# Performance work log

Measured on AMD Instinct MI355X. Metric: run time of the kernel, lower is better.

Reference implementation:

```python
import jax, jax.numpy as jnp
import numpy as np

B, S, D = 4, 1024, 1024
H = 16
HD = D // H  # 64
LN_EPS = 1e-5


def setup_inputs() -> dict:
    key = jax.random.key(0)
    ks = jax.random.split(key, 12)
    s = 1.0 / np.sqrt(D)
    return {
        "x": jax.random.normal(ks[0], (B, S, D), dtype=jnp.float32),
        "wq": jax.random.normal(ks[1], (D, D), dtype=jnp.float32) * s,
        "bq": jnp.zeros((D,), dtype=jnp.float32),
        "wk": jax.random.normal(ks[2], (D, D), dtype=jnp.float32) * s,
        "bk": jnp.zeros((D,), dtype=jnp.float32),
        "wv": jax.random.normal(ks[3], (D, D), dtype=jnp.float32) * s,
        "bv": jnp.zeros((D,), dtype=jnp.float32),
        "wl": jax.random.normal(ks[4], (D, D), dtype=jnp.float32) * s,
        "bl": jnp.zeros((D,), dtype=jnp.float32),
        "ln_g": jnp.ones((D,), dtype=jnp.float32),
        "ln_b": jnp.zeros((D,), dtype=jnp.float32),
    }


def _heads(t):
    # [B,S,D] -> [B,H,S,HD]
    return t.reshape(B, S, H, HD).transpose(0, 2, 1, 3)


def reference(x, wq, bq, wk, bk, wv, bv, wl, bl, ln_g, ln_b):
    q = _heads(x @ wq.T + bq)
    k = _heads(x @ wk.T + bk)
    v = _heads(x @ wv.T + bv)
    score = jnp.einsum("bhqd,bhkd->bhqk", q, k)
    # NOTE: unusual order — softmax first, THEN divide by sqrt(head_size)
    score = jax.nn.softmax(score, axis=-1) / jnp.sqrt(jnp.float32(HD))
    att = jnp.einsum("bhqk,bhkd->bhqd", score, v)
    att = att.transpose(0, 2, 1, 3).reshape(B, S, D)
    # residual added BEFORE the output linear
    y = (att + x) @ wl.T + bl
    # LayerNorm over last dim
    mu = jnp.mean(y, axis=-1, keepdims=True)
    var = jnp.mean(jnp.square(y - mu), axis=-1, keepdims=True)
    out = (y - mu) * jax.lax.rsqrt(var + LN_EPS) * ln_g + ln_b
    # dropout is identity in eval mode
    return out
```

## Files before the change

### kernel.cpp

```cpp
#include <hip/hip_runtime.h>
#include <cstdint>
#include <cstddef>

typedef __bf16 bf16;
typedef __bf16 bf16x4_t __attribute__((ext_vector_type(4)));
typedef __bf16 bf16x8_t __attribute__((ext_vector_type(8)));
typedef float f32x4_t __attribute__((ext_vector_type(4)));

#define DEV static __device__ __forceinline__

DEV void gload16(const void* g, void* l) {
  __builtin_amdgcn_global_load_lds((const __attribute__((address_space(1))) void*)g,
                                   (__attribute__((address_space(3))) void*)l, 16, 0, 0);
}

DEV f32x4_t mfma16(bf16x8_t a, bf16x8_t b, f32x4_t c) {
  return __builtin_amdgcn_mfma_f32_16x16x32_bf16(a, b, c, 0, 0, 0);
}

__global__ __launch_bounds__(256) void k_convert(
    const float* __restrict__ x, const float* __restrict__ wq,
    const float* __restrict__ wk, const float* __restrict__ wv,
    const float* __restrict__ wl,
    bf16* __restrict__ xb, bf16* __restrict__ wqkvb, bf16* __restrict__ wlb) {
  const size_t M1 = (size_t)1 << 20;
  size_t i = ((size_t)blockIdx.x * 256 + threadIdx.x) * 4;
  const float* src; bf16* dst; size_t off;
  if (i < 4 * M1)      { src = x;  dst = xb;           off = i; }
  else if (i < 5 * M1) { src = wq; dst = wqkvb;        off = i - 4 * M1; }
  else if (i < 6 * M1) { src = wk; dst = wqkvb + M1;   off = i - 5 * M1; }
  else if (i < 7 * M1) { src = wv; dst = wqkvb + 2*M1; off = i - 6 * M1; }
  else                 { src = wl; dst = wlb;          off = i - 7 * M1; }
  f32x4_t v = *(const f32x4_t*)&src[off];
  bf16x4_t o;
  o[0] = (bf16)v[0]; o[1] = (bf16)v[1]; o[2] = (bf16)v[2]; o[3] = (bf16)v[3];
  *(bf16x4_t*)&dst[off] = o;
}

DEV void gemm_mainloop(const bf16* __restrict__ A, const bf16* __restrict__ B,
                       int m0, int n0,
                       bf16 (*lA)[128 * 64], bf16 (*lB)[128 * 64],
                       f32x4_t (&acc)[4][4]) {
  const int tid = threadIdx.x, wave = tid >> 6, lane = tid & 63;
  const int wm = (wave >> 1) * 64, wn = (wave & 1) * 64;
  const int fr = lane & 15, fg = lane >> 4;
  const int rowoff = wave * 8 + (lane >> 3);
  const int csw = (((lane & 7) ^ (lane >> 3)) << 3);

  auto STAGE = [&](int buf, int kt) {
#pragma unroll
    for (int i = 0; i < 4; ++i) {
      gload16(A + (size_t)(m0 + i * 32 + rowoff) * 1024 + kt * 64 + csw,
              &lA[buf][(i * 32 + wave * 8) * 64]);
      gload16(B + (size_t)(n0 + i * 32 + rowoff) * 1024 + kt * 64 + csw,
              &lB[buf][(i * 32 + wave * 8) * 64]);
    }
  };

  auto COMPUTE = [&](int buf) {
    bf16x8_t af[4][2], bfr[4][2];
#pragma unroll
    for (int mi = 0; mi < 4; ++mi)
#pragma unroll
      for (int ks = 0; ks < 2; ++ks) {
        const int r = wm + mi * 16 + fr;
        af[mi][ks] = *(const bf16x8_t*)
            &lA[buf][r * 64 + ((((ks << 2) + fg) ^ (fr & 7)) << 3)];
      }
#pragma unroll
    for (int ni = 0; ni < 4; ++ni)
#pragma unroll
      for (int ks = 0; ks < 2; ++ks) {
        const int r = wn + ni * 16 + fr;
        bfr[ni][ks] = *(const bf16x8_t*)
            &lB[buf][r * 64 + ((((ks << 2) + fg) ^ (fr & 7)) << 3)];
      }
    __builtin_amdgcn_s_setprio(1);
#pragma unroll
    for (int ks = 0; ks < 2; ++ks)
#pragma unroll
      for (int mi = 0; mi < 4; ++mi)
#pragma unroll
        for (int ni = 0; ni < 4; ++ni)
          acc[mi][ni] = mfma16(af[mi][ks], bfr[ni][ks], acc[mi][ni]);
    __builtin_amdgcn_s_setprio(0);
  };

  STAGE(0, 0);
  STAGE(1, 1);
  for (int t = 0; t < 15; ++t) {
    asm volatile("s_waitcnt vmcnt(8)" ::: "memory");
    __builtin_amdgcn_s_barrier();
    COMPUTE(t & 1);
    __builtin_amdgcn_s_barrier();
    if (t < 14) STAGE(t & 1, t + 2);
  }
  asm volatile("s_waitcnt vmcnt(0)" ::: "memory");
  __builtin_amdgcn_s_barrier();
  COMPUTE(1);
}

__global__ __launch_bounds__(256, 2) void k_gemm_qkv(
    const bf16* __restrict__ W, const bf16* __restrict__ Xb,
    const float* __restrict__ bq, const float* __restrict__ bk,
    const float* __restrict__ bv,
    bf16* __restrict__ Q, bf16* __restrict__ Kc, bf16* __restrict__ VT) {
  __shared__ alignas(16) bf16 lA[2][128 * 64];
  __shared__ alignas(16) bf16 lB[2][128 * 64];
  const f32x4_t vzero = {0.f, 0.f, 0.f, 0.f};
  f32x4_t acc[4][4];
#pragma unroll
  for (int a = 0; a < 4; ++a)
#pragma unroll
    for (int c = 0; c < 4; ++c) acc[a][c] = vzero;
  const int m0 = blockIdx.x * 128, n0 = blockIdx.y * 128;
  gemm_mainloop(W, Xb, m0, n0, lA, lB, acc);

  const int tid = threadIdx.x, wave = tid >> 6, lane = tid & 63;
  const int wm = (wave >> 1) * 64, wn = (wave & 1) * 64;
  const int fr = lane & 15, fg = lane >> 4;
  const int region = m0 >> 10;
  const float* bp = (region == 0) ? bq : ((region == 1) ? bk : bv);
  bf16* QK = (region == 0) ? Q : Kc;
#pragma unroll
  for (int mi = 0; mi < 4; ++mi) {
    const int f = (m0 & 1023) + wm + mi * 16 + fg * 4;
    const int h = f >> 6, d = f & 63;
#pragma unroll
    for (int ni = 0; ni < 4; ++ni) {
      const int t = n0 + wn + ni * 16 + fr;
      const int b = t >> 10, s = t & 1023;
      const int bh = b * 16 + h;
      f32x4_t v = acc[mi][ni];
      if (region < 2) {
        bf16x4_t o;
#pragma unroll
        for (int j = 0; j < 4; ++j) o[j] = (bf16)(v[j] + bp[f + j]);
        *(bf16x4_t*)&QK[((size_t)bh * 1024 + s) * 64 + d] = o;
      } else {
#pragma unroll
        for (int j = 0; j < 4; ++j)
          VT[((size_t)bh * 64 + d + j) * 1024 + s] = (bf16)(v[j] + bp[f + j]);
      }
    }
  }
}

#define P_STRIDE 72

__global__ __launch_bounds__(256) void k_attn(
    const bf16* __restrict__ Q, const bf16* __restrict__ K,
    const bf16* __restrict__ VT, const float* __restrict__ X,
    bf16* __restrict__ ATTB) {
  __shared__ alignas(16) bf16 lK[2][64 * 64];
  __shared__ alignas(16) bf16 lV[2][64 * 64];
  __shared__ alignas(16) bf16 lP[4][32 * P_STRIDE];
  const int tid = threadIdx.x, wave = tid >> 6, lane = tid & 63;
  const int bh = blockIdx.x, qt = blockIdx.y;
  const int q0 = qt * 128 + wave * 32;
  const int fr = lane & 15, fg = lane >> 4;
  const int rx = (fr & 7) << 3;
  const f32x4_t vzero = {0.f, 0.f, 0.f, 0.f};

  bf16x8_t qf[2][2];
#pragma unroll
  for (int mi = 0; mi < 2; ++mi)
#pragma unroll
    for (int ks = 0; ks < 2; ++ks)
      qf[mi][ks] = *(const bf16x8_t*)
          &Q[((size_t)bh * 1024 + q0 + mi * 16 + fr) * 64 + ks * 32 + fg * 8];

  f32x4_t oacc[2][4];
  f32x4_t lsum[2];
#pragma unroll
  for (int mi = 0; mi < 2; ++mi) {
    lsum[mi] = vzero;
#pragma unroll
    for (int dj = 0; dj < 4; ++dj) oacc[mi][dj] = vzero;
  }

  const int srow = lane >> 3;
  const int scolsw = (((lane & 7) ^ srow) * 8);

  auto STAGE = [&](int buf, int kv) {
#pragma unroll
    for (int i = 0; i < 2; ++i) {
      const int c = wave * 2 + i;
      gload16(&K[((size_t)bh * 1024 + kv * 64 + c * 8 + srow) * 64 + scolsw],
              &lK[buf][c * 512]);
      gload16(&VT[((size_t)bh * 64 + c * 8 + srow) * 1024 + kv * 64 + scolsw],
              &lV[buf][c * 512]);
    }
  };

  STAGE(0, 0);
  __syncthreads();

  for (int kv = 0; kv < 16; ++kv) {
    const int cur = kv & 1;
    if (kv < 15) STAGE(cur ^ 1, kv + 1);

    bf16x8_t kb[4][2];
#pragma unroll
    for (int nj = 0; nj < 4; ++nj)
#pragma unroll
      for (int ks = 0; ks < 2; ++ks) {
        const int r = nj * 16 + fr;
        kb[nj][ks] = *(const bf16x8_t*)&lK[cur][r * 64 + ((ks * 32 + fg * 8) ^ rx)];
      }
    f32x4_t s[2][4];
#pragma unroll
    for (int mi = 0; mi < 2; ++mi)
#pragma unroll
      for (int nj = 0; nj < 4; ++nj) {
        f32x4_t z = vzero;
#pragma unroll
        for (int ks = 0; ks < 2; ++ks) z = mfma16(qf[mi][ks], kb[nj][ks], z);
        s[mi][nj] = z;
      }

#pragma unroll
    for (int mi = 0; mi < 2; ++mi)
#pragma unroll
      for (int nj = 0; nj < 4; ++nj)
#pragma unroll
        for (int j = 0; j < 4; ++j) {
          float p = __expf(s[mi][nj][j]);
          lsum[mi][j] += p;
          lP[wave][(mi * 16 + fg * 4 + j) * P_STRIDE + nj * 16 + fr] = (bf16)p;
        }

    bf16x8_t vb[4][2], pa[2][2];
#pragma unroll
    for (int dj = 0; dj < 4; ++dj)
#pragma unroll
      for (int ks = 0; ks < 2; ++ks) {
        const int r = dj * 16 + fr;
        vb[dj][ks] = *(const bf16x8_t*)&lV[cur][r * 64 + ((ks * 32 + fg * 8) ^ rx)];
      }
#pragma unroll
    for (int mi = 0; mi < 2; ++mi)
#pragma unroll
      for (int ks = 0; ks < 2; ++ks)
        pa[mi][ks] = *(const bf16x8_t*)
            &lP[wave][(mi * 16 + fr) * P_STRIDE + ks * 32 + fg * 8];
#pragma unroll
    for (int mi = 0; mi < 2; ++mi)
#pragma unroll
      for (int dj = 0; dj < 4; ++dj)
#pragma unroll
        for (int ks = 0; ks < 2; ++ks)
          oacc[mi][dj] = mfma16(pa[mi][ks], vb[dj][ks], oacc[mi][dj]);

    __syncthreads();
  }

#pragma unroll
  for (int mi = 0; mi < 2; ++mi)
#pragma unroll
    for (int m = 1; m < 16; m <<= 1)
#pragma unroll
      for (int j = 0; j < 4; ++j)
        lsum[mi][j] += __shfl_xor(lsum[mi][j], m);

  const int b = bh >> 4, h = bh & 15;
#pragma unroll
  for (int mi = 0; mi < 2; ++mi)
#pragma unroll
    for (int dj = 0; dj < 4; ++dj)
#pragma unroll
      for (int j = 0; j < 4; ++j) {
        const int s_ = q0 + mi * 16 + fg * 4 + j;
        const int d_ = dj * 16 + fr;
        const size_t tok = (size_t)b * 1024 + s_;
        const size_t fidx = (size_t)h * 64 + d_;
        float val = oacc[mi][dj][j] / lsum[mi][j] * 0.125f + X[tok * 1024 + fidx];
        ATTB[tok * 1024 + fidx] = (bf16)val;
      }
}

__global__ __launch_bounds__(256, 2) void k_gemm_out(
    const bf16* __restrict__ Wl, const bf16* __restrict__ Ax,
    const float* __restrict__ bl, float* __restrict__ Y) {
  __shared__ alignas(16) bf16 lA[2][128 * 64];
  __shared__ alignas(16) bf16 lB[2][128 * 64];
  const f32x4_t vzero = {0.f, 0.f, 0.f, 0.f};
  f32x4_t acc[4][4];
#pragma unroll
  for (int a = 0; a < 4; ++a)
#pragma unroll
    for (int c = 0; c < 4; ++c) acc[a][c] = vzero;
  const int m0 = blockIdx.x * 128, n0 = blockIdx.y * 128;
  gemm_mainloop(Wl, Ax, m0, n0, lA, lB, acc);

  const int tid = threadIdx.x, wave = tid >> 6, lane = tid & 63;
  const int wm = (wave >> 1) * 64, wn = (wave & 1) * 64;
  const int fr = lane & 15, fg = lane >> 4;
#pragma unroll
  for (int mi = 0; mi < 4; ++mi) {
    const int f = m0 + wm + mi * 16 + fg * 4;
#pragma unroll
    for (int ni = 0; ni < 4; ++ni) {
      const int t = n0 + wn + ni * 16 + fr;
      f32x4_t v = acc[mi][ni], o;
#pragma unroll
      for (int j = 0; j < 4; ++j) o[j] = v[j] + bl[f + j];
      *(f32x4_t*)&Y[(size_t)t * 1024 + f] = o;
    }
  }
}

__global__ __launch_bounds__(256) void k_ln(
    const float* __restrict__ Y, const float* __restrict__ g,
    const float* __restrict__ bta, float* __restrict__ OUT) {
  const int row = blockIdx.x, tid = threadIdx.x;
  const float* y = Y + (size_t)row * 1024;
  f32x4_t v = *(const f32x4_t*)&y[tid * 4];
  float s = v[0] + v[1] + v[2] + v[3];
  float s2 = v[0]*v[0] + v[1]*v[1] + v[2]*v[2] + v[3]*v[3];
#pragma unroll
  for (int m = 1; m < 64; m <<= 1) {
    s += __shfl_xor(s, m);
    s2 += __shfl_xor(s2, m);
  }
  __shared__ float ps[4], ps2[4];
  const int wave = tid >> 6, lane = tid & 63;
  if (lane == 0) { ps[wave] = s; ps2[wave] = s2; }
  __syncthreads();
  s = ps[0] + ps[1] + ps[2] + ps[3];
  s2 = ps2[0] + ps2[1] + ps2[2] + ps2[3];
  const float mu = s * (1.f / 1024.f);
  const float var = s2 * (1.f / 1024.f) - mu * mu;
  const float rs = rsqrtf(var + 1e-5f);
  f32x4_t gg = *(const f32x4_t*)&g[tid * 4];
  f32x4_t bb = *(const f32x4_t*)&bta[tid * 4];
  f32x4_t o;
#pragma unroll
  for (int j = 0; j < 4; ++j) o[j] = (v[j] - mu) * rs * gg[j] + bb[j];
  *(f32x4_t*)&OUT[(size_t)row * 1024 + tid * 4] = o;
}

extern "C" void kernel_launch(void* const* d_in, const int* in_sizes, int n_in,
                              void* d_out, int out_size, void* d_ws, size_t ws_size,
                              hipStream_t stream) {
  (void)in_sizes; (void)n_in; (void)out_size; (void)ws_size;
  const float* x   = (const float*)d_in[0];
  const float* wq  = (const float*)d_in[1];
  const float* bq  = (const float*)d_in[2];
  const float* wk  = (const float*)d_in[3];
  const float* bk  = (const float*)d_in[4];
  const float* wv  = (const float*)d_in[5];
  const float* bv  = (const float*)d_in[6];
  const float* wl  = (const float*)d_in[7];
  const float* bl  = (const float*)d_in[8];
  const float* lng = (const float*)d_in[9];
  const float* lnb = (const float*)d_in[10];

  const size_t MB = (size_t)1 << 20;
  char* ws = (char*)d_ws;
  bf16* xb    = (bf16*)(ws);
  bf16* wqkvb = (bf16*)(ws + 8 * MB);
  bf16* wlb   = (bf16*)(ws + 14 * MB);
  bf16* Qb    = (bf16*)(ws + 16 * MB);
  bf16* Kb    = (bf16*)(ws + 24 * MB);
  bf16* VTb   = (bf16*)(ws + 32 * MB);
  bf16* attb  = (bf16*)(ws + 40 * MB);
  float* Y    = (float*)(ws + 16 * MB);

  k_convert<<<dim3(8192), dim3(256), 0, stream>>>(x, wq, wk, wv, wl, xb, wqkvb, wlb);
  k_gemm_qkv<<<dim3(24, 32), dim3(256), 0, stream>>>(wqkvb, xb, bq, bk, bv, Qb, Kb, VTb);
  k_attn<<<dim3(64, 8), dim3(256), 0, stream>>>(Qb, Kb, VTb, x, attb);
  k_gemm_out<<<dim3(8, 32), dim3(256), 0, stream>>>(wlb, attb, bl, Y);
  k_ln<<<dim3(4096), dim3(256), 0, stream>>>(Y, lng, lnb, (float*)d_out);
}
```

Before: 114.5 us.

## Rewrite QKV GEMM with 256x256 tiles, 8 waves, and quartered prefetch pipeline

Replaces the 128x128, 4-wave QKV projection GEMM with a 256x256-tile, 512-thread kernel. Each wave computes a 128x64 sub-tile in four quadrant phases, with global-to-LDS prefetches for the next k-steps interleaved between the phases. The larger tile is meant to raise LDS data reuse per MFMA and to hide load latency more finely. In exchange it uses more LDS and registers, and the grid drops to 192 blocks, which may leave some compute units underused.

```diff
diff --git a/kernel.cpp b/kernel.cpp
--- a/kernel.cpp
+++ b/kernel.cpp
@@ -17,6 +17,12 @@
 DEV f32x4_t mfma16(bf16x8_t a, bf16x8_t b, f32x4_t c) {
   return __builtin_amdgcn_mfma_f32_16x16x32_bf16(a, b, c, 0, 0, 0);
 }
+
+#define BAR __builtin_amdgcn_s_barrier()
+#define FENCE asm volatile("" ::: "memory")
+#define LGKM0 do { asm volatile("s_waitcnt lgkmcnt(0)" ::: "memory"); \
+                   __builtin_amdgcn_sched_barrier(0); } while (0)
+#define VMC(n) asm volatile("s_waitcnt vmcnt(" #n ")" ::: "memory")
 
 __global__ __launch_bounds__(256) void k_convert(
     const float* __restrict__ x, const float* __restrict__ wq,
@@ -37,6 +43,153 @@
   *(bf16x4_t*)&dst[off] = o;
 }
 
+__global__ __launch_bounds__(512, 2) void k_gemm_qkv(
+    const bf16* __restrict__ W, const bf16* __restrict__ Xb,
+    const float* __restrict__ bq, const float* __restrict__ bk,
+    const float* __restrict__ bv,
+    bf16* __restrict__ Q, bf16* __restrict__ Kc, bf16* __restrict__ VT) {
+  __shared__ alignas(16) bf16 lA[2][256 * 64];
+  __shared__ alignas(16) bf16 lB[2][256 * 64];
+  const int tid = threadIdx.x, w = tid >> 6, lane = tid & 63;
+  const int wr = w >> 2, wc = w & 3;
+  const int fr = lane & 15, fg = lane >> 4;
+  const int srow = lane >> 3;
+  const int csw = (((lane & 7) ^ srow) << 3);
+  const int m0 = blockIdx.x * 256, n0 = blockIdx.y * 256;
+
+  f32x4_t acc[8][4];
+  const f32x4_t vzero = {0.f, 0.f, 0.f, 0.f};
+#pragma unroll
+  for (int a = 0; a < 8; ++a)
+#pragma unroll
+    for (int c = 0; c < 4; ++c) acc[a][c] = vzero;
+
+  auto SA = [&](int buf, int kt, int row0) {
+    gload16(W + (size_t)(m0 + row0 + srow) * 1024 + kt * 64 + csw,
+            &lA[buf][row0 * 64]);
+  };
+  auto SB = [&](int buf, int kt, int row0) {
+    gload16(Xb + (size_t)(n0 + row0 + srow) * 1024 + kt * 64 + csw,
+            &lB[buf][row0 * 64]);
+  };
+  const int a0 = w * 8;
+  const int b0 = (w >> 2) * 64 + (w & 3) * 8;
+
+  bf16x8_t af[4][2], bfr[4][2];
+
+  auto LDA = [&](int buf, int qm) {
+#pragma unroll
+    for (int mi = 0; mi < 4; ++mi)
+#pragma unroll
+      for (int ks = 0; ks < 2; ++ks) {
+        const int r = wr * 128 + qm * 64 + mi * 16 + fr;
+        af[mi][ks] = *(const bf16x8_t*)
+            &lA[buf][r * 64 + ((((ks << 2) + fg) ^ (r & 7)) << 3)];
+      }
+  };
+  auto LDB = [&](int buf, int qn) {
+#pragma unroll
+    for (int i = 0; i < 2; ++i)
+#pragma unroll
+      for (int ks = 0; ks < 2; ++ks) {
+        const int r = wc * 64 + (qn * 2 + i) * 16 + fr;
+        bfr[qn * 2 + i][ks] = *(const bf16x8_t*)
+            &lB[buf][r * 64 + ((((ks << 2) + fg) ^ (r & 7)) << 3)];
+      }
+  };
+  auto MM = [&](int qm, int qn) {
+    __builtin_amdgcn_s_setprio(1);
+#pragma unroll
+    for (int ks = 0; ks < 2; ++ks)
+#pragma unroll
+      for (int mi = 0; mi < 4; ++mi)
+#pragma unroll
+        for (int i = 0; i < 2; ++i)
+          acc[qm * 4 + mi][qn * 2 + i] =
+              mfma16(af[mi][ks], bfr[qn * 2 + i][ks], acc[qm * 4 + mi][qn * 2 + i]);
+    __builtin_amdgcn_s_setprio(0);
+  };
+
+  SA(0, 0, a0); SA(0, 0, a0 + 64); SA(0, 0, a0 + 128); SA(0, 0, a0 + 192);
+  SB(0, 0, a0); SB(0, 0, a0 + 64); SB(0, 0, a0 + 128); SB(0, 0, a0 + 192);
+  SA(1, 1, a0); SA(1, 1, a0 + 128);
+  SB(1, 1, b0); SB(1, 1, b0 + 128);
+  SB(1, 1, b0 + 32); SB(1, 1, b0 + 160);
+  VMC(6); BAR; FENCE;
+
+#pragma unroll 2
+  for (int t = 0; t < 14; ++t) {
+    const int p = t & 1;
+    LDA(p, 0); LDB(p, 0);
+    SA(p ^ 1, t + 1, a0 + 64); SA(p ^ 1, t + 1, a0 + 192);
+    BAR; FENCE; LGKM0;
+    MM(0, 0);
+    BAR; FENCE;
+    LDB(p, 1);
+    SA(p, t + 2, a0); SA(p, t + 2, a0 + 128);
+    BAR; FENCE; LGKM0;
+    MM(0, 1);
+    BAR; FENCE;
+    LDA(p, 1);
+    SB(p, t + 2, b0); SB(p, t + 2, b0 + 128);
+    BAR; FENCE; LGKM0;
+    MM(1, 0);
+    BAR; FENCE;
+    SB(p, t + 2, b0 + 32); SB(p, t + 2, b0 + 160);
+    BAR; FENCE;
+    MM(1, 1);
+    VMC(6);
+    BAR; FENCE;
+  }
+  {
+    LDA(0, 0); LDB(0, 0);
+    SA(1, 15, a0 + 64); SA(1, 15, a0 + 192);
+    BAR; FENCE; LGKM0; MM(0, 0); BAR; FENCE;
+    LDB(0, 1);
+    BAR; FENCE; LGKM0; MM(0, 1); BAR; FENCE;
+    LDA(0, 1);
+    BAR; FENCE; LGKM0; MM(1, 0); BAR; FENCE;
+    MM(1, 1);
+    VMC(0);
+    BAR; FENCE;
+  }
+  {
+    LDA(1, 0); LDB(1, 0);
+    BAR; FENCE; LGKM0; MM(0, 0); BAR; FENCE;
+    LDB(1, 1);
+    BAR; FENCE; LGKM0; MM(0, 1); BAR; FENCE;
+    LDA(1, 1);
+    BAR; FENCE; LGKM0; MM(1, 0); BAR; FENCE;
+    MM(1, 1);
+  }
+
+  const int region = m0 >> 10;
+  const float* bp = (region == 0) ? bq : ((region == 1) ? bk : bv);
+  bf16* QK = (region == 0) ? Q : Kc;
+#pragma unroll
+  for (int mi = 0; mi < 8; ++mi) {
+    const int f = (m0 & 1023) + wr * 128 + mi * 16 + fg * 4;
+    const int h = f >> 6, d = f & 63;
+#pragma unroll
+    for (int ni = 0; ni < 4; ++ni) {
+      const int tkn = n0 + wc * 64 + ni * 16 + fr;
+      const int b = tkn >> 10, s = tkn & 1023;
+      const int bh = b * 16 + h;
+      f32x4_t v = acc[mi][ni];
+      if (region < 2) {
+        bf16x4_t o;
+#pragma unroll
+        for (int j = 0; j < 4; ++j) o[j] = (bf16)(v[j] + bp[f + j]);
+        *(bf16x4_t*)&QK[((size_t)bh * 1024 + s) * 64 + d] = o;
+      } else {
+#pragma unroll
+        for (int j = 0; j < 4; ++j)
+          VT[((size_t)bh * 64 + d + j) * 1024 + s] = (bf16)(v[j] + bp[f + j]);
+      }
+    }
+  }
+}
+
 DEV void gemm_mainloop(const bf16* __restrict__ A, const bf16* __restrict__ B,
                        int m0, int n0,
                        bf16 (*lA)[128 * 64], bf16 (*lB)[128 * 64],
@@ -98,52 +251,6 @@
   asm volatile("s_waitcnt vmcnt(0)" ::: "memory");
   __builtin_amdgcn_s_barrier();
   COMPUTE(1);
-}
-
-__global__ __launch_bounds__(256, 2) void k_gemm_qkv(
-    const bf16* __restrict__ W, const bf16* __restrict__ Xb,
-    const float* __restrict__ bq, const float* __restrict__ bk,
-    const float* __restrict__ bv,
-    bf16* __restrict__ Q, bf16* __restrict__ Kc, bf16* __restrict__ VT) {
-  __shared__ alignas(16) bf16 lA[2][128 * 64];
-  __shared__ alignas(16) bf16 lB[2][128 * 64];
-  const f32x4_t vzero = {0.f, 0.f, 0.f, 0.f};
-  f32x4_t acc[4][4];
-#pragma unroll
-  for (int a = 0; a < 4; ++a)
-#pragma unroll
-    for (int c = 0; c < 4; ++c) acc[a][c] = vzero;
-  const int m0 = blockIdx.x * 128, n0 = blockIdx.y * 128;
-  gemm_mainloop(W, Xb, m0, n0, lA, lB, acc);
-
-  const int tid = threadIdx.x, wave = tid >> 6, lane = tid & 63;
-  const int wm = (wave >> 1) * 64, wn = (wave & 1) * 64;
-  const int fr = lane & 15, fg = lane >> 4;
-  const int region = m0 >> 10;
-  const float* bp = (region == 0) ? bq : ((region == 1) ? bk : bv);
-  bf16* QK = (region == 0) ? Q : Kc;
-#pragma unroll
-  for (int mi = 0; mi < 4; ++mi) {
-    const int f = (m0 & 1023) + wm + mi * 16 + fg * 4;
-    const int h = f >> 6, d = f & 63;
-#pragma unroll
-    for (int ni = 0; ni < 4; ++ni) {
-      const int t = n0 + wn + ni * 16 + fr;
-      const int b = t >> 10, s = t & 1023;
-      const int bh = b * 16 + h;
-      f32x4_t v = acc[mi][ni];
-      if (region < 2) {
-        bf16x4_t o;
-#pragma unroll
-        for (int j = 0; j < 4; ++j) o[j] = (bf16)(v[j] + bp[f + j]);
-        *(bf16x4_t*)&QK[((size_t)bh * 1024 + s) * 64 + d] = o;
-      } else {
-#pragma unroll
-        for (int j = 0; j < 4; ++j)
-          VT[((size_t)bh * 64 + d + j) * 1024 + s] = (bf16)(v[j] + bp[f + j]);
-      }
-    }
-  }
 }
 
 #define P_STRIDE 72
@@ -368,7 +475,7 @@
   float* Y    = (float*)(ws + 16 * MB);
 
   k_convert<<<dim3(8192), dim3(256), 0, stream>>>(x, wq, wk, wv, wl, xb, wqkvb, wlb);
-  k_gemm_qkv<<<dim3(24, 32), dim3(256), 0, stream>>>(wqkvb, xb, bq, bk, bv, Qb, Kb, VTb);
+  k_gemm_qkv<<<dim3(12, 16), dim3(512), 0, stream>>>(wqkvb, xb, bq, bk, bv, Qb, Kb, VTb);
   k_attn<<<dim3(64, 8), dim3(256), 0, stream>>>(Qb, Kb, VTb, x, attb);
   k_gemm_out<<<dim3(8, 32), dim3(256), 0, stream>>>(wlb, attb, bl, Y);
   k_ln<<<dim3(4096), dim3(256), 0, stream>>>(Y, lng, lnb, (float*)d_out);
```

Result: faster. 111.9 us (-2.2%).

## Coalesce V-transpose stores via LDS and deepen attention K/V prefetch

Applied to the files above, without the earlier changes.

The QKV GEMM is rewritten as a single-buffered LDS loop instead of the shared double-buffered mainloop, and the occupancy hint is dropped. For the V region, the epilogue now transposes the tile through swizzled shared memory and writes VT with 16-byte coalesced stores, replacing scattered 2-byte stores. The attention kernel now prefetches K/V two tiles ahead, using explicit vmcnt waits and barriers in place of a per-iteration __syncthreads. The risk is that the single-buffered GEMM exposes global load latency that double buffering used to hide.

```diff
diff --git a/kernel.cpp b/kernel.cpp
--- a/kernel.cpp
+++ b/kernel.cpp
@@ -17,6 +17,10 @@
 DEV f32x4_t mfma16(bf16x8_t a, bf16x8_t b, f32x4_t c) {
   return __builtin_amdgcn_mfma_f32_16x16x32_bf16(a, b, c, 0, 0, 0);
 }
+
+#define BAR __builtin_amdgcn_s_barrier()
+#define FENCE asm volatile("" ::: "memory")
+#define VMC(n) asm volatile("s_waitcnt vmcnt(" #n ")" ::: "memory")
 
 __global__ __launch_bounds__(256) void k_convert(
     const float* __restrict__ x, const float* __restrict__ wq,
@@ -37,6 +41,118 @@
   *(bf16x4_t*)&dst[off] = o;
 }
 
+__global__ __launch_bounds__(256) void k_gemm_qkv(
+    const bf16* __restrict__ W, const bf16* __restrict__ Xb,
+    const float* __restrict__ bq, const float* __restrict__ bk,
+    const float* __restrict__ bv,
+    bf16* __restrict__ Q, bf16* __restrict__ Kc, bf16* __restrict__ VT) {
+  __shared__ alignas(16) bf16 smem[16384];
+  bf16* lA = smem;
+  bf16* lB = smem + 8192;
+  const int tid = threadIdx.x, wave = tid >> 6, lane = tid & 63;
+  const int wm = (wave >> 1) * 64, wn = (wave & 1) * 64;
+  const int fr = lane & 15, fg = lane >> 4;
+  const int csw = (((lane & 7) ^ (lane >> 3)) << 3);
+  const int m0 = blockIdx.x * 128, n0 = blockIdx.y * 128;
+
+  f32x4_t acc[4][4];
+  const f32x4_t vzero = {0.f, 0.f, 0.f, 0.f};
+#pragma unroll
+  for (int a = 0; a < 4; ++a)
+#pragma unroll
+    for (int c = 0; c < 4; ++c) acc[a][c] = vzero;
+
+  const int rowoff = wave * 8 + (lane >> 3);
+
+  for (int kt = 0; kt < 16; ++kt) {
+#pragma unroll
+    for (int i = 0; i < 4; ++i) {
+      gload16(W + (size_t)(m0 + i * 32 + rowoff) * 1024 + kt * 64 + csw,
+              &lA[(i * 32 + wave * 8) * 64]);
+      gload16(Xb + (size_t)(n0 + i * 32 + rowoff) * 1024 + kt * 64 + csw,
+              &lB[(i * 32 + wave * 8) * 64]);
+    }
+    __syncthreads();
+    bf16x8_t af[4][2], bfr[4][2];
+#pragma unroll
+    for (int mi = 0; mi < 4; ++mi)
+#pragma unroll
+      for (int ks = 0; ks < 2; ++ks) {
+        const int r = wm + mi * 16 + fr;
+        af[mi][ks] = *(const bf16x8_t*)
+            &lA[r * 64 + ((((ks << 2) + fg) ^ (fr & 7)) << 3)];
+      }
+#pragma unroll
+    for (int ni = 0; ni < 4; ++ni)
+#pragma unroll
+      for (int ks = 0; ks < 2; ++ks) {
+        const int r = wn + ni * 16 + fr;
+        bfr[ni][ks] = *(const bf16x8_t*)
+            &lB[r * 64 + ((((ks << 2) + fg) ^ (fr & 7)) << 3)];
+      }
+    __builtin_amdgcn_s_setprio(1);
+#pragma unroll
+    for (int ks = 0; ks < 2; ++ks)
+#pragma unroll
+      for (int mi = 0; mi < 4; ++mi)
+#pragma unroll
+        for (int ni = 0; ni < 4; ++ni)
+          acc[mi][ni] = mfma16(af[mi][ks], bfr[ni][ks], acc[mi][ni]);
+    __builtin_amdgcn_s_setprio(0);
+    __syncthreads();
+  }
+
+  const int region = m0 >> 10;
+  const float* bp = (region == 0) ? bq : ((region == 1) ? bk : bv);
+  if (region < 2) {
+    bf16* QK = (region == 0) ? Q : Kc;
+#pragma unroll
+    for (int mi = 0; mi < 4; ++mi) {
+      const int f = (m0 & 1023) + wm + mi * 16 + fg * 4;
+      const int h = f >> 6, d = f & 63;
+#pragma unroll
+      for (int ni = 0; ni < 4; ++ni) {
+        const int t = n0 + wn + ni * 16 + fr;
+        const int b = t >> 10, s = t & 1023;
+        const int bh = b * 16 + h;
+        f32x4_t v = acc[mi][ni];
+        bf16x4_t o;
+#pragma unroll
+        for (int j = 0; j < 4; ++j) o[j] = (bf16)(v[j] + bp[f + j]);
+        *(bf16x4_t*)&QK[((size_t)bh * 1024 + s) * 64 + d] = o;
+      }
+    }
+  } else {
+#pragma unroll
+    for (int mi = 0; mi < 4; ++mi) {
+      const int dl = wm + mi * 16 + fg * 4;
+      const int floc = (m0 & 1023) + dl;
+#pragma unroll
+      for (int ni = 0; ni < 4; ++ni) {
+        const int sl = wn + ni * 16 + fr;
+        f32x4_t v = acc[mi][ni];
+#pragma unroll
+        for (int j = 0; j < 4; ++j) {
+          const int d = dl + j;
+          smem[d * 128 + (sl ^ ((d & 7) << 3))] = (bf16)(v[j] + bp[floc + j]);
+        }
+      }
+    }
+    __syncthreads();
+    const int b = n0 >> 10;
+#pragma unroll
+    for (int i = 0; i < 8; ++i) {
+      const int d = i * 16 + (tid >> 4);
+      const int c = tid & 15;
+      bf16x8_t vv = *(const bf16x8_t*)&smem[d * 128 + ((c ^ (d & 7)) << 3)];
+      const int floc = (m0 & 1023) + d;
+      const int h = floc >> 6, dd = floc & 63;
+      const int sg = (n0 & 1023) + c * 8;
+      *(bf16x8_t*)&VT[((size_t)(b * 16 + h) * 64 + dd) * 1024 + sg] = vv;
+    }
+  }
+}
+
 DEV void gemm_mainloop(const bf16* __restrict__ A, const bf16* __restrict__ B,
                        int m0, int n0,
                        bf16 (*lA)[128 * 64], bf16 (*lB)[128 * 64],
@@ -98,52 +214,6 @@
   asm volatile("s_waitcnt vmcnt(0)" ::: "memory");
   __builtin_amdgcn_s_barrier();
   COMPUTE(1);
-}
-
-__global__ __launch_bounds__(256, 2) void k_gemm_qkv(
-    const bf16* __restrict__ W, const bf16* __restrict__ Xb,
-    const float* __restrict__ bq, const float* __restrict__ bk,
-    const float* __restrict__ bv,
-    bf16* __restrict__ Q, bf16* __restrict__ Kc, bf16* __restrict__ VT) {
-  __shared__ alignas(16) bf16 lA[2][128 * 64];
-  __shared__ alignas(16) bf16 lB[2][128 * 64];
-  const f32x4_t vzero = {0.f, 0.f, 0.f, 0.f};
-  f32x4_t acc[4][4];
-#pragma unroll
-  for (int a = 0; a < 4; ++a)
-#pragma unroll
-    for (int c = 0; c < 4; ++c) acc[a][c] = vzero;
-  const int m0 = blockIdx.x * 128, n0 = blockIdx.y * 128;
-  gemm_mainloop(W, Xb, m0, n0, lA, lB, acc);
-
-  const int tid = threadIdx.x, wave = tid >> 6, lane = tid & 63;
-  const int wm = (wave >> 1) * 64, wn = (wave & 1) * 64;
-  const int fr = lane & 15, fg = lane >> 4;
-  const int region = m0 >> 10;
-  const float* bp = (region == 0) ? bq : ((region == 1) ? bk : bv);
-  bf16* QK = (region == 0) ? Q : Kc;
-#pragma unroll
-  for (int mi = 0; mi < 4; ++mi) {
-    const int f = (m0 & 1023) + wm + mi * 16 + fg * 4;
-    const int h = f >> 6, d = f & 63;
-#pragma unroll
-    for (int ni = 0; ni < 4; ++ni) {
-      const int t = n0 + wn + ni * 16 + fr;
-      const int b = t >> 10, s = t & 1023;
-      const int bh = b * 16 + h;
-      f32x4_t v = acc[mi][ni];
-      if (region < 2) {
-        bf16x4_t o;
-#pragma unroll
-        for (int j = 0; j < 4; ++j) o[j] = (bf16)(v[j] + bp[f + j]);
-        *(bf16x4_t*)&QK[((size_t)bh * 1024 + s) * 64 + d] = o;
-      } else {
-#pragma unroll
-        for (int j = 0; j < 4; ++j)
-          VT[((size_t)bh * 64 + d + j) * 1024 + s] = (bf16)(v[j] + bp[f + j]);
-      }
-    }
-  }
 }
 
 #define P_STRIDE 72
@@ -193,13 +263,7 @@
     }
   };
 
-  STAGE(0, 0);
-  __syncthreads();
-
-  for (int kv = 0; kv < 16; ++kv) {
-    const int cur = kv & 1;
-    if (kv < 15) STAGE(cur ^ 1, kv + 1);
-
+  auto TILE = [&](int cur) {
     bf16x8_t kb[4][2];
 #pragma unroll
     for (int nj = 0; nj < 4; ++nj)
@@ -251,9 +315,18 @@
 #pragma unroll
         for (int ks = 0; ks < 2; ++ks)
           oacc[mi][dj] = mfma16(pa[mi][ks], vb[dj][ks], oacc[mi][dj]);
-
-    __syncthreads();
-  }
+  };
+
+  STAGE(0, 0);
+  STAGE(1, 1);
+  for (int kv = 0; kv < 15; ++kv) {
+    VMC(4); BAR; FENCE;
+    TILE(kv & 1);
+    BAR; FENCE;
+    if (kv < 14) STAGE(kv & 1, kv + 2);
+  }
+  VMC(0); BAR; FENCE;
+  TILE(1);
 
 #pragma unroll
   for (int mi = 0; mi < 2; ++mi)
```

Measured after the change: 113.1 us. About the same (-1.2%).
